# Optimization experiments

Hardware: AMD Instinct MI355X
Metric: run time of the kernel (lower is better)

Reference implementation:

```python
import jax, jax.numpy as jnp
import numpy as np

B, N = 2, 2048
D_MODEL, HEADS = 512, 8
D_K = D_MODEL // HEADS
D_HIDDEN = 2048
MIN_SPREAD = 2.0
MIN_RBF = 1e-3
MAX_RBF = 1.0
LN_EPS = 1e-5


def setup_inputs() -> dict:
    key = jax.random.key(0)
    ks = jax.random.split(key, 12)
    xs = (6.0 / (D_K + D_MODEL)) ** 0.5
    q = jax.random.normal(ks[0], (B, N, D_MODEL), dtype=jnp.float32)
    k = jax.random.normal(ks[1], (B, N, D_MODEL), dtype=jnp.float32)
    v = jax.random.normal(ks[2], (B, N, D_MODEL), dtype=jnp.float32)
    coords = jax.random.normal(ks[3], (B, N, 3), dtype=jnp.float32) * 10.0
    mask = jnp.ones((B, N), dtype=bool)
    q_proj = jax.random.uniform(ks[4], (HEADS, D_MODEL, D_K), minval=-xs, maxval=xs)
    k_proj = jax.random.uniform(ks[5], (HEADS, D_MODEL, D_K), minval=-xs, maxval=xs)
    v_proj = jax.random.uniform(ks[6], (HEADS, D_MODEL, D_K), minval=-xs, maxval=xs)
    q_bias = jnp.zeros((HEADS, D_K))
    k_bias = jnp.zeros((HEADS, D_K))
    v_bias = jnp.zeros((HEADS, D_K))
    ow = (1.0 / D_MODEL) ** 0.5
    out_w = jax.random.uniform(ks[7], (D_MODEL, D_MODEL), minval=-ow, maxval=ow)
    spread_w = jnp.zeros((HEADS,))
    beta_w = jnp.zeros((HEADS,))
    ln1_g = jnp.ones((D_MODEL,)); ln1_b = jnp.zeros((D_MODEL,))
    ln2_g = jnp.ones((D_MODEL,)); ln2_b = jnp.zeros((D_MODEL,))
    w1 = jax.random.normal(ks[8], (D_MODEL, D_HIDDEN)) * 0.02
    b1 = jnp.zeros((D_HIDDEN,))
    w2 = jax.random.normal(ks[9], (D_HIDDEN, D_MODEL)) * 0.02
    b2 = jnp.zeros((D_MODEL,))
    return dict(q=q, k=k, v=v, coords=coords, mask=mask,
                q_proj=q_proj, k_proj=k_proj, v_proj=v_proj,
                q_bias=q_bias, k_bias=k_bias, v_bias=v_bias,
                out_w=out_w, spread_w=spread_w, beta_w=beta_w,
                ln1_g=ln1_g, ln1_b=ln1_b, ln2_g=ln2_g, ln2_b=ln2_b,
                w1=w1, b1=b1, w2=w2, b2=b2)


def _layernorm(x, g, b):
    mu = jnp.mean(x, axis=-1, keepdims=True)
    var = jnp.mean((x - mu) ** 2, axis=-1, keepdims=True)
    return (x - mu) * jax.lax.rsqrt(var + LN_EPS) * g + b


def _geo_attention(q, k, v, coords, mask,
                   q_proj, k_proj, v_proj, q_bias, k_bias, v_bias,
                   out_w, spread_w, beta_w):
    # per-head projections: [B,H,N,dk]
    Q = jnp.einsum('bnd,hdk->bhnk', q, q_proj) + q_bias[None, :, None, :]
    K = jnp.einsum('bnd,hdk->bhnk', k, k_proj) + k_bias[None, :, None, :]
    V = jnp.einsum('bnd,hdk->bhnk', v, v_proj) + v_bias[None, :, None, :]

    spreads = MIN_SPREAD + jnp.exp(spread_w)   # [H]
    betas = jnp.exp(beta_w)                    # [H]

    # pairwise squared distances [B,N,N]
    d2 = jnp.sum((coords[:, :, None, :] - coords[:, None, :, :]) ** 2, axis=-1)
    # per-head Gaussian RBF [B,H,N,N]
    rbf = jnp.exp(-d2[:, None, :, :] / (2.0 * spreads[None, :, None, None] ** 2))

    scores = jnp.einsum('bhnk,bhmk->bhnm', Q, K) / jnp.sqrt(jnp.float32(D_K))
    scores = betas[None, :, None, None] * rbf * scores

    # sparsity: keys with rbf outside [min_rbf, max_rbf] or padded are masked out
    valid = (rbf >= MIN_RBF) & (rbf <= MAX_RBF) & mask[:, None, None, :]
    scores = jnp.where(valid, scores, -jnp.inf)
    attn = jax.nn.softmax(scores, axis=-1)     # diagonal always valid (rbf=1)

    out = jnp.einsum('bhnm,bhmk->bhnk', attn, V)         # [B,H,N,dk]
    # torch: out.permute(0,2,3,1).reshape(B,N,d_model) -> (b,n,dk,h) layout
    out = jnp.transpose(out, (0, 2, 3, 1)).reshape(out.shape[0], out.shape[2], D_MODEL)
    return out @ out_w.T


def reference(q, k, v, coords, mask,
              q_proj, k_proj, v_proj, q_bias, k_bias, v_bias,
              out_w, spread_w, beta_w,
              ln1_g, ln1_b, ln2_g, ln2_b, w1, b1, w2, b2):
    attn_out = _geo_attention(q, k, v, coords, mask,
                              q_proj, k_proj, v_proj, q_bias, k_bias, v_bias,
                              out_w, spread_w, beta_w)
    x = _layernorm(q + attn_out, ln1_g, ln1_b)
    ffn = jax.nn.relu(x @ w1 + b1) @ w2 + b2
    x = _layernorm(x + ffn, ln2_g, ln2_b)
    return x
```

## Files before the change

### kernel.cpp

```cpp
#include <hip/hip_runtime.h>
#include <math.h>

typedef __attribute__((ext_vector_type(8))) short bf16x8;
typedef __attribute__((ext_vector_type(4))) float f32x4;

#define MFMA16(a,b,c) __builtin_amdgcn_mfma_f32_16x16x32_bf16((a),(b),(c),0,0,0)

__device__ __forceinline__ unsigned short f2bf(float f) {
    union { float f; unsigned u; } x; x.f = f;
    unsigned r = x.u + 0x7FFFu + ((x.u >> 16) & 1u);
    return (unsigned short)(r >> 16);
}

__device__ __forceinline__ unsigned cvt_pk_bf16(float lo, float hi) {
    unsigned r;
    asm("v_cvt_pk_bf16_f32 %0, %1, %2" : "=v"(r) : "v"(lo), "v"(hi));
    return r;
}

__global__ __launch_bounds__(256) void cvt_qkv(
    const float* __restrict__ q, const float* __restrict__ k,
    const float* __restrict__ v,
    unsigned short* __restrict__ qb, unsigned short* __restrict__ kb,
    unsigned short* __restrict__ vb, int n)
{
    for (int i = blockIdx.x * 256 + threadIdx.x; i < n; i += gridDim.x * 256) {
        qb[i] = f2bf(q[i]); kb[i] = f2bf(k[i]); vb[i] = f2bf(v[i]);
    }
}

__global__ __launch_bounds__(256) void cvt_weights(
    const float* __restrict__ qp, const float* __restrict__ kp,
    const float* __restrict__ vp, const float* __restrict__ ow,
    const float* __restrict__ w1, const float* __restrict__ w2,
    unsigned short* __restrict__ qpT, unsigned short* __restrict__ kpT,
    unsigned short* __restrict__ vpT, unsigned short* __restrict__ owT,
    unsigned short* __restrict__ w1T, unsigned short* __restrict__ w2T)
{
    const int NP = 262144;
    const int total = 4 * NP + 1048576 + 1048576;
    for (int i = blockIdx.x * 256 + threadIdx.x; i < total; i += gridDim.x * 256) {
        if (i < 3 * NP) {
            int which = i / NP, r = i - which * NP;
            int n = r >> 9, d = r & 511;
            int h = n >> 6, kk = n & 63;
            const float* src = (which == 0) ? qp : (which == 1) ? kp : vp;
            unsigned short* dst = (which == 0) ? qpT : (which == 1) ? kpT : vpT;
            dst[r] = f2bf(src[(h << 15) + (d << 6) + kk]);
        } else if (i < 4 * NP) {
            int r = i - 3 * NP;
            int oi = r >> 9, f = r & 511;
            int h = f >> 6, kk = f & 63;
            owT[r] = f2bf(ow[(oi << 9) + (kk << 3) + h]);
        } else if (i < 4 * NP + 1048576) {
            int r = i - 4 * NP;
            int n = r >> 9, d = r & 511;
            w1T[r] = f2bf(w1[(d << 11) + n]);
        } else {
            int r = i - 4 * NP - 1048576;
            int n = r >> 11, d = r & 2047;
            w2T[r] = f2bf(w2[(d << 9) + n]);
        }
    }
}

template<int RELU, int SF32, int SB16, int SVTR>
__global__ __launch_bounds__(256) void gemm_bt(
    const unsigned short* __restrict__ A,
    const unsigned short* __restrict__ Bt,
    const float* __restrict__ bias,
    float* __restrict__ Cf, unsigned short* __restrict__ Cb,
    int M, int N, int K)
{
    __shared__ unsigned short As[128][72];
    __shared__ unsigned short Bs[128][72];
    const int tid = threadIdx.x;
    const int m0 = blockIdx.y << 7, n0 = blockIdx.x << 7;
    const int wv = tid >> 6, lane = tid & 63;
    const int lrow = lane & 15, kg = lane >> 4;
    const int wr = (wv >> 1) << 6, wc = (wv & 1) << 6;

    f32x4 acc[4][4];
    const f32x4 z4 = {0.f, 0.f, 0.f, 0.f};
#pragma unroll
    for (int i = 0; i < 4; ++i)
#pragma unroll
        for (int j = 0; j < 4; ++j) acc[i][j] = z4;

    const int nkt = K >> 6;
    for (int kt = 0; kt < nkt; ++kt) {
        __syncthreads();
        const int k0 = kt << 6;
#pragma unroll
        for (int i = 0; i < 4; ++i) {
            int slot = tid + (i << 8);
            int r = slot >> 3, c = (slot & 7) << 3;
            *(int4*)(&As[r][c]) = *(const int4*)(&A[(long)(m0 + r) * K + k0 + c]);
            *(int4*)(&Bs[r][c]) = *(const int4*)(&Bt[(long)(n0 + r) * K + k0 + c]);
        }
        __syncthreads();
#pragma unroll
        for (int ks = 0; ks < 2; ++ks) {
            const int koff = (ks << 5) + (kg << 3);
            bf16x8 af[4], bfr[4];
#pragma unroll
            for (int mi = 0; mi < 4; ++mi)
                af[mi] = *(const bf16x8*)(&As[wr + (mi << 4) + lrow][koff]);
#pragma unroll
            for (int ni = 0; ni < 4; ++ni)
                bfr[ni] = *(const bf16x8*)(&Bs[wc + (ni << 4) + lrow][koff]);
#pragma unroll
            for (int mi = 0; mi < 4; ++mi)
#pragma unroll
                for (int ni = 0; ni < 4; ++ni)
                    acc[mi][ni] = MFMA16(af[mi], bfr[ni], acc[mi][ni]);
        }
    }

#pragma unroll
    for (int mi = 0; mi < 4; ++mi) {
#pragma unroll
        for (int ni = 0; ni < 4; ++ni) {
            const int col = n0 + wc + (ni << 4) + lrow;
            const float bv = bias ? bias[col] : 0.0f;
#pragma unroll
            for (int j = 0; j < 4; ++j) {
                const int row = m0 + wr + (mi << 4) + (kg << 2) + j;
                float val = acc[mi][ni][j] + bv;
                if (RELU) val = fmaxf(val, 0.0f);
                if (SF32) Cf[(long)row * N + col] = val;
                if (SB16) Cb[(long)row * N + col] = f2bf(val);
                if (SVTR)
                    Cb[((long)(row >> 11) << 20) + ((long)col << 11) + (row & 2047)] = f2bf(val);
            }
        }
    }
}

__global__ __launch_bounds__(256) void geo_attn(
    const unsigned short* __restrict__ Qh,
    const unsigned short* __restrict__ Kh,
    const unsigned short* __restrict__ VhT,
    const float* __restrict__ coords,
    const float* __restrict__ spread_w, const float* __restrict__ beta_w,
    unsigned short* __restrict__ Ob)
{
    __shared__ unsigned short Qs[64][72];
    __shared__ unsigned short Ks[64][72];
    __shared__ unsigned short Vs[64][72];
    __shared__ unsigned short Ps[4][16][72];
    __shared__ float4 ck4[64];

    const int tid = threadIdx.x;
    const int bid = blockIdx.x;
    const int swz = ((bid & 7) << 6) + (bid >> 3);
    const int bh = swz >> 5, qt = swz & 31;
    const int b = bh >> 3, h = bh & 7;
    const int wv = tid >> 6, lane = tid & 63;
    const int lq = lane & 15, kg = lane >> 4;
    const float NEG_INF = -__builtin_inff();

    const float spread = 2.0f + __expf(spread_w[h]);
    const float inv2s2 = 1.0f / (2.0f * spread * spread);
    const float coef = __expf(beta_w[h]) * 0.125f;

    {
        const long qbase = ((long)(b * 2048 + qt * 64)) * 512 + h * 64;
#pragma unroll
        for (int i = 0; i < 2; ++i) {
            int slot = tid + (i << 8);
            int r = slot >> 3, c = (slot & 7) << 3;
            *(int4*)(&Qs[r][c]) = *(const int4*)(&Qh[qbase + (long)r * 512 + c]);
        }
    }

    float cqx, cqy, cqz;
    {
        long ca = ((long)(b * 2048 + qt * 64 + wv * 16 + lq)) * 3;
        cqx = coords[ca]; cqy = coords[ca + 1]; cqz = coords[ca + 2];
    }

    float mrun = NEG_INF, lrun = 0.0f;
    f32x4 Oa[4];
    const f32x4 z4 = {0.f, 0.f, 0.f, 0.f};
#pragma unroll
    for (int nd = 0; nd < 4; ++nd) Oa[nd] = z4;

    const long kbase0 = ((long)b * 2048) * 512 + h * 64;
    const long vbase = ((long)(b * 8 + h)) * 131072;

    for (int kt = 0; kt < 32; ++kt) {
        __syncthreads();
        const int k0 = kt << 6;
#pragma unroll
        for (int i = 0; i < 2; ++i) {
            int slot = tid + (i << 8);
            int r = slot >> 3, c = (slot & 7) << 3;
            *(int4*)(&Ks[r][c]) = *(const int4*)(&Kh[kbase0 + (long)(k0 + r) * 512 + c]);
            *(int4*)(&Vs[r][c]) = *(const int4*)(&VhT[vbase + (long)r * 2048 + k0 + c]);
        }
        if (tid < 64) {
            long ca = ((long)(b * 2048 + k0 + tid)) * 3;
            ck4[tid] = make_float4(coords[ca], coords[ca + 1], coords[ca + 2], 0.0f);
        }
        __syncthreads();

        f32x4 t4[4];
#pragma unroll
        for (int ra = 0; ra < 4; ++ra) t4[ra] = z4;
#pragma unroll
        for (int ks = 0; ks < 2; ++ks) {
            const int koff = (ks << 5) + (kg << 3);
            bf16x8 bq = *(const bf16x8*)(&Qs[(wv << 4) + lq][koff]);
#pragma unroll
            for (int ra = 0; ra < 4; ++ra) {
                bf16x8 ak = *(const bf16x8*)(&Ks[(ra << 4) + lq][koff]);
                t4[ra] = MFMA16(ak, bq, t4[ra]);
            }
        }

        float tmax = NEG_INF;
#pragma unroll
        for (int ra = 0; ra < 4; ++ra) {
#pragma unroll
            for (int j = 0; j < 4; ++j) {
                float4 ck = ck4[(ra << 4) + (kg << 2) + j];
                float dx = cqx - ck.x, dy = cqy - ck.y, dz = cqz - ck.z;
                float d2 = dx * dx + dy * dy + dz * dz;
                float rbf = __expf(-d2 * inv2s2);
                float val = (rbf >= 1e-3f) ? coef * rbf * t4[ra][j] : NEG_INF;
                t4[ra][j] = val;
                tmax = fmaxf(tmax, val);
            }
        }
        tmax = fmaxf(tmax, __shfl_xor(tmax, 16, 64));
        tmax = fmaxf(tmax, __shfl_xor(tmax, 32, 64));

        const float mn = fmaxf(mrun, tmax);
        const bool dead = (mn == NEG_INF);
        const float mneff = dead ? 0.0f : mn;
        const float fcorr = dead ? 1.0f : __expf(mrun - mn);

        float psum = 0.0f;
#pragma unroll
        for (int ra = 0; ra < 4; ++ra) {
#pragma unroll
            for (int j = 0; j < 4; ++j) {
                float p = __expf(t4[ra][j] - mneff);
                t4[ra][j] = p;
                psum += p;
            }
        }
        psum += __shfl_xor(psum, 16, 64);
        psum += __shfl_xor(psum, 32, 64);
        mrun = mn;
        lrun = lrun * fcorr + psum;

#pragma unroll
        for (int ra = 0; ra < 4; ++ra) {
            uint2 pk;
            pk.x = cvt_pk_bf16(t4[ra][0], t4[ra][1]);
            pk.y = cvt_pk_bf16(t4[ra][2], t4[ra][3]);
            *(uint2*)(&Ps[wv][lq][(ra << 4) + (kg << 2)]) = pk;
        }

        float fb[4];
#pragma unroll
        for (int j = 0; j < 4; ++j)
            fb[j] = __shfl(fcorr, (lane & 48) | ((kg << 2) + j), 64);
#pragma unroll
        for (int nd = 0; nd < 4; ++nd)
#pragma unroll
            for (int j = 0; j < 4; ++j)
                Oa[nd][j] *= fb[j];

#pragma unroll
        for (int ks = 0; ks < 2; ++ks) {
            const int koff = (ks << 5) + (kg << 3);
            bf16x8 ap = *(const bf16x8*)(&Ps[wv][lq][koff]);
#pragma unroll
            for (int nd = 0; nd < 4; ++nd) {
                bf16x8 bv = *(const bf16x8*)(&Vs[(nd << 4) + lq][koff]);
                Oa[nd] = MFMA16(ap, bv, Oa[nd]);
            }
        }
    }

    const float inv = 1.0f / lrun;
    float il[4];
#pragma unroll
    for (int j = 0; j < 4; ++j)
        il[j] = __shfl(inv, (lane & 48) | ((kg << 2) + j), 64);
    const long obase = ((long)(b * 2048 + qt * 64 + (wv << 4))) * 512 + h * 64;
#pragma unroll
    for (int nd = 0; nd < 4; ++nd)
#pragma unroll
        for (int j = 0; j < 4; ++j)
            Ob[obase + (long)((kg << 2) + j) * 512 + (nd << 4) + lq] =
                f2bf(Oa[nd][j] * il[j]);
}

template<int SB16>
__global__ __launch_bounds__(256) void ln_res(
    const float* __restrict__ X, const float* __restrict__ R,
    const float* __restrict__ g, const float* __restrict__ bb,
    float* __restrict__ Yf, unsigned short* __restrict__ Yb)
{
    const int wv = threadIdx.x >> 6, lane = threadIdx.x & 63;
    const long row = (long)blockIdx.x * 4 + wv;
    const float* xp = X + row * 512;
    const float* rp = R + row * 512;
    const int c0 = lane * 8;
    float4 a0 = *(const float4*)(xp + c0);
    float4 a1 = *(const float4*)(xp + c0 + 4);
    float4 r0 = *(const float4*)(rp + c0);
    float4 r1 = *(const float4*)(rp + c0 + 4);
    float v[8] = {a0.x + r0.x, a0.y + r0.y, a0.z + r0.z, a0.w + r0.w,
                  a1.x + r1.x, a1.y + r1.y, a1.z + r1.z, a1.w + r1.w};
    float s = 0.f, ss = 0.f;
#pragma unroll
    for (int i = 0; i < 8; ++i) { s += v[i]; ss += v[i] * v[i]; }
#pragma unroll
    for (int off = 1; off < 64; off <<= 1) {
        s += __shfl_xor(s, off, 64);
        ss += __shfl_xor(ss, off, 64);
    }
    const float mu = s * (1.0f / 512.0f);
    const float var = ss * (1.0f / 512.0f) - mu * mu;
    const float rstd = rsqrtf(var + 1e-5f);
#pragma unroll
    for (int i = 0; i < 8; ++i) {
        const int c = c0 + i;
        const float y = (v[i] - mu) * rstd * g[c] + bb[c];
        Yf[row * 512 + c] = y;
        if (SB16) Yb[row * 512 + c] = f2bf(y);
    }
}

extern "C" void kernel_launch(void* const* d_in, const int* in_sizes, int n_in,
                              void* d_out, int out_size, void* d_ws, size_t ws_size,
                              hipStream_t stream)
{
    const float* q      = (const float*)d_in[0];
    const float* k      = (const float*)d_in[1];
    const float* v      = (const float*)d_in[2];
    const float* coords = (const float*)d_in[3];
    const float* q_proj = (const float*)d_in[5];
    const float* k_proj = (const float*)d_in[6];
    const float* v_proj = (const float*)d_in[7];
    const float* q_bias = (const float*)d_in[8];
    const float* k_bias = (const float*)d_in[9];
    const float* v_bias = (const float*)d_in[10];
    const float* out_w  = (const float*)d_in[11];
    const float* spread_w = (const float*)d_in[12];
    const float* beta_w = (const float*)d_in[13];
    const float* ln1_g  = (const float*)d_in[14];
    const float* ln1_b  = (const float*)d_in[15];
    const float* ln2_g  = (const float*)d_in[16];
    const float* ln2_b  = (const float*)d_in[17];
    const float* w1     = (const float*)d_in[18];
    const float* b1     = (const float*)d_in[19];
    const float* w2     = (const float*)d_in[20];
    const float* b2     = (const float*)d_in[21];
    float* out = (float*)d_out;

    char* ws = (char*)d_ws;
    size_t off = 0;
    auto alloc = [&](size_t bytes) -> void* {
        void* p = ws + off;
        off += (bytes + 255) & ~(size_t)255;
        return p;
    };
    unsigned short* qb   = (unsigned short*)alloc(4096UL * 512 * 2);
    unsigned short* kb   = (unsigned short*)alloc(4096UL * 512 * 2);
    unsigned short* vb   = (unsigned short*)alloc(4096UL * 512 * 2);
    unsigned short* qpT  = (unsigned short*)alloc(512UL * 512 * 2);
    unsigned short* kpT  = (unsigned short*)alloc(512UL * 512 * 2);
    unsigned short* vpT  = (unsigned short*)alloc(512UL * 512 * 2);
    unsigned short* owT  = (unsigned short*)alloc(512UL * 512 * 2);
    unsigned short* w1T  = (unsigned short*)alloc(2048UL * 512 * 2);
    unsigned short* w2T  = (unsigned short*)alloc(512UL * 2048 * 2);
    unsigned short* Qp   = (unsigned short*)alloc(4096UL * 512 * 2);
    unsigned short* Kp   = (unsigned short*)alloc(4096UL * 512 * 2);
    unsigned short* VpT  = (unsigned short*)alloc(4096UL * 512 * 2);
    unsigned short* attnb= (unsigned short*)alloc(4096UL * 512 * 2);
    float* proj = (float*)alloc(4096UL * 512 * 4);
    float* x1   = (float*)alloc(4096UL * 512 * 4);
    unsigned short* x1b = (unsigned short*)alloc(4096UL * 512 * 2);
    unsigned short* hid = (unsigned short*)alloc(4096UL * 2048 * 2);
    float* ffn  = (float*)alloc(4096UL * 512 * 4);
    (void)ws_size; (void)in_sizes; (void)n_in; (void)out_size;

    cvt_qkv<<<2048, 256, 0, stream>>>(q, k, v, qb, kb, vb, 2097152);
    cvt_weights<<<2048, 256, 0, stream>>>(q_proj, k_proj, v_proj, out_w, w1, w2,
                                          qpT, kpT, vpT, owT, w1T, w2T);

    dim3 g512(4, 32);
    gemm_bt<0, 0, 1, 0><<<g512, 256, 0, stream>>>(qb, qpT, q_bias, nullptr, Qp, 4096, 512, 512);
    gemm_bt<0, 0, 1, 0><<<g512, 256, 0, stream>>>(kb, kpT, k_bias, nullptr, Kp, 4096, 512, 512);
    gemm_bt<0, 0, 0, 1><<<g512, 256, 0, stream>>>(vb, vpT, v_bias, nullptr, VpT, 4096, 512, 512);

    geo_attn<<<512, 256, 0, stream>>>(Qp, Kp, VpT, coords, spread_w, beta_w, attnb);

    gemm_bt<0, 1, 0, 0><<<g512, 256, 0, stream>>>(attnb, owT, nullptr, proj, nullptr, 4096, 512, 512);
    ln_res<1><<<1024, 256, 0, stream>>>(proj, q, ln1_g, ln1_b, x1, x1b);

    dim3 g2048(16, 32);
    gemm_bt<1, 0, 1, 0><<<g2048, 256, 0, stream>>>(x1b, w1T, b1, nullptr, hid, 4096, 2048, 512);
    gemm_bt<0, 1, 0, 0><<<g512, 256, 0, stream>>>(hid, w2T, b2, ffn, nullptr, 4096, 512, 2048);
    ln_res<0><<<1024, 256, 0, stream>>>(ffn, x1, ln2_g, ln2_b, out, nullptr);
}
```

Baseline: 229.6 us.

## Fuse fp32-to-bf16 input conversion into GEMMs, add register prefetch, widen attention tiles

Drops the separate q/k/v conversion kernel. The projection GEMMs now read fp32 activations directly and convert them while staging into shared memory. GEMM and attention loops prefetch the next tile into registers while computing on the current one. The GEMM M-tile becomes a template parameter, set to 64 for the 512-wide GEMMs to launch more blocks. Attention processes 128 keys per iteration with Q held in registers, halving the loop count, at the cost of more registers and LDS, which may lower occupancy.

```diff
diff --git a/kernel.cpp b/kernel.cpp
--- a/kernel.cpp
+++ b/kernel.cpp
@@ -16,17 +16,6 @@
     unsigned r;
     asm("v_cvt_pk_bf16_f32 %0, %1, %2" : "=v"(r) : "v"(lo), "v"(hi));
     return r;
-}
-
-__global__ __launch_bounds__(256) void cvt_qkv(
-    const float* __restrict__ q, const float* __restrict__ k,
-    const float* __restrict__ v,
-    unsigned short* __restrict__ qb, unsigned short* __restrict__ kb,
-    unsigned short* __restrict__ vb, int n)
-{
-    for (int i = blockIdx.x * 256 + threadIdx.x; i < n; i += gridDim.x * 256) {
-        qb[i] = f2bf(q[i]); kb[i] = f2bf(k[i]); vb[i] = f2bf(v[i]);
-    }
 }
 
 __global__ __launch_bounds__(256) void cvt_weights(
@@ -64,61 +53,105 @@
     }
 }
 
-template<int RELU, int SF32, int SB16, int SVTR>
+template<int TM, int AF32, int RELU, int SF32, int SB16, int SVTR>
 __global__ __launch_bounds__(256) void gemm_bt(
-    const unsigned short* __restrict__ A,
+    const void* __restrict__ Av,
     const unsigned short* __restrict__ Bt,
     const float* __restrict__ bias,
     float* __restrict__ Cf, unsigned short* __restrict__ Cb,
     int M, int N, int K)
 {
-    __shared__ unsigned short As[128][72];
+    constexpr int AC = TM / 32;
+    __shared__ unsigned short As[TM][72];
     __shared__ unsigned short Bs[128][72];
     const int tid = threadIdx.x;
-    const int m0 = blockIdx.y << 7, n0 = blockIdx.x << 7;
+    const int m0 = blockIdx.y * TM, n0 = blockIdx.x << 7;
     const int wv = tid >> 6, lane = tid & 63;
     const int lrow = lane & 15, kg = lane >> 4;
-    const int wr = (wv >> 1) << 6, wc = (wv & 1) << 6;
-
-    f32x4 acc[4][4];
+    const int wr = (wv >> 1) * (TM / 2), wc = (wv & 1) << 6;
+
+    f32x4 acc[AC][4];
     const f32x4 z4 = {0.f, 0.f, 0.f, 0.f};
 #pragma unroll
-    for (int i = 0; i < 4; ++i)
+    for (int i = 0; i < AC; ++i)
 #pragma unroll
         for (int j = 0; j < 4; ++j) acc[i][j] = z4;
 
+    float4 arf[AC][2];
+    int4 arb[AC];
+    int4 br[4];
+
+    auto loadT = [&](int kt) {
+        const int k0 = kt << 6;
+#pragma unroll
+        for (int i = 0; i < AC; ++i) {
+            int slot = tid + (i << 8);
+            int r = slot >> 3, c = (slot & 7) << 3;
+            if (AF32) {
+                const float* Af = (const float*)Av;
+                arf[i][0] = *(const float4*)(&Af[(long)(m0 + r) * K + k0 + c]);
+                arf[i][1] = *(const float4*)(&Af[(long)(m0 + r) * K + k0 + c + 4]);
+            } else {
+                const unsigned short* Ab = (const unsigned short*)Av;
+                arb[i] = *(const int4*)(&Ab[(long)(m0 + r) * K + k0 + c]);
+            }
+        }
+#pragma unroll
+        for (int i = 0; i < 4; ++i) {
+            int slot = tid + (i << 8);
+            int r = slot >> 3, c = (slot & 7) << 3;
+            br[i] = *(const int4*)(&Bt[(long)(n0 + r) * K + k0 + c]);
+        }
+    };
+    auto writeT = [&]() {
+#pragma unroll
+        for (int i = 0; i < AC; ++i) {
+            int slot = tid + (i << 8);
+            int r = slot >> 3, c = (slot & 7) << 3;
+            if (AF32) {
+                int4 w;
+                w.x = (int)cvt_pk_bf16(arf[i][0].x, arf[i][0].y);
+                w.y = (int)cvt_pk_bf16(arf[i][0].z, arf[i][0].w);
+                w.z = (int)cvt_pk_bf16(arf[i][1].x, arf[i][1].y);
+                w.w = (int)cvt_pk_bf16(arf[i][1].z, arf[i][1].w);
+                *(int4*)(&As[r][c]) = w;
+            } else {
+                *(int4*)(&As[r][c]) = arb[i];
+            }
+        }
+#pragma unroll
+        for (int i = 0; i < 4; ++i) {
+            int slot = tid + (i << 8);
+            *(int4*)(&Bs[slot >> 3][(slot & 7) << 3]) = br[i];
+        }
+    };
+
     const int nkt = K >> 6;
+    loadT(0); writeT(); __syncthreads();
+
     for (int kt = 0; kt < nkt; ++kt) {
-        __syncthreads();
-        const int k0 = kt << 6;
-#pragma unroll
-        for (int i = 0; i < 4; ++i) {
-            int slot = tid + (i << 8);
-            int r = slot >> 3, c = (slot & 7) << 3;
-            *(int4*)(&As[r][c]) = *(const int4*)(&A[(long)(m0 + r) * K + k0 + c]);
-            *(int4*)(&Bs[r][c]) = *(const int4*)(&Bt[(long)(n0 + r) * K + k0 + c]);
-        }
-        __syncthreads();
+        if (kt + 1 < nkt) loadT(kt + 1);
 #pragma unroll
         for (int ks = 0; ks < 2; ++ks) {
             const int koff = (ks << 5) + (kg << 3);
-            bf16x8 af[4], bfr[4];
-#pragma unroll
-            for (int mi = 0; mi < 4; ++mi)
+            bf16x8 af[AC], bfr[4];
+#pragma unroll
+            for (int mi = 0; mi < AC; ++mi)
                 af[mi] = *(const bf16x8*)(&As[wr + (mi << 4) + lrow][koff]);
 #pragma unroll
             for (int ni = 0; ni < 4; ++ni)
                 bfr[ni] = *(const bf16x8*)(&Bs[wc + (ni << 4) + lrow][koff]);
 #pragma unroll
-            for (int mi = 0; mi < 4; ++mi)
+            for (int mi = 0; mi < AC; ++mi)
 #pragma unroll
                 for (int ni = 0; ni < 4; ++ni)
                     acc[mi][ni] = MFMA16(af[mi], bfr[ni], acc[mi][ni]);
         }
-    }
-
-#pragma unroll
-    for (int mi = 0; mi < 4; ++mi) {
+        if (kt + 1 < nkt) { __syncthreads(); writeT(); __syncthreads(); }
+    }
+
+#pragma unroll
+    for (int mi = 0; mi < AC; ++mi) {
 #pragma unroll
         for (int ni = 0; ni < 4; ++ni) {
             const int col = n0 + wc + (ni << 4) + lrow;
@@ -145,11 +178,10 @@
     const float* __restrict__ spread_w, const float* __restrict__ beta_w,
     unsigned short* __restrict__ Ob)
 {
-    __shared__ unsigned short Qs[64][72];
-    __shared__ unsigned short Ks[64][72];
-    __shared__ unsigned short Vs[64][72];
-    __shared__ unsigned short Ps[4][16][72];
-    __shared__ float4 ck4[64];
+    __shared__ unsigned short Ks[128][72];
+    __shared__ unsigned short Vs[64][136];
+    __shared__ unsigned short Ps[4][16][136];
+    __shared__ float4 ck4[128];
 
     const int tid = threadIdx.x;
     const int bid = blockIdx.x;
@@ -164,21 +196,11 @@
     const float inv2s2 = 1.0f / (2.0f * spread * spread);
     const float coef = __expf(beta_w[h]) * 0.125f;
 
-    {
-        const long qbase = ((long)(b * 2048 + qt * 64)) * 512 + h * 64;
-#pragma unroll
-        for (int i = 0; i < 2; ++i) {
-            int slot = tid + (i << 8);
-            int r = slot >> 3, c = (slot & 7) << 3;
-            *(int4*)(&Qs[r][c]) = *(const int4*)(&Qh[qbase + (long)r * 512 + c]);
-        }
-    }
-
+    const long qrow = (long)(b * 2048 + qt * 64 + wv * 16 + lq);
+    const bf16x8 qA = *(const bf16x8*)(&Qh[qrow * 512 + h * 64 + (kg << 3)]);
+    const bf16x8 qB = *(const bf16x8*)(&Qh[qrow * 512 + h * 64 + 32 + (kg << 3)]);
     float cqx, cqy, cqz;
-    {
-        long ca = ((long)(b * 2048 + qt * 64 + wv * 16 + lq)) * 3;
-        cqx = coords[ca]; cqy = coords[ca + 1]; cqz = coords[ca + 2];
-    }
+    { long ca = qrow * 3; cqx = coords[ca]; cqy = coords[ca + 1]; cqz = coords[ca + 2]; }
 
     float mrun = NEG_INF, lrun = 0.0f;
     f32x4 Oa[4];
@@ -189,31 +211,48 @@
     const long kbase0 = ((long)b * 2048) * 512 + h * 64;
     const long vbase = ((long)(b * 8 + h)) * 131072;
 
-    for (int kt = 0; kt < 32; ++kt) {
-        __syncthreads();
-        const int k0 = kt << 6;
-#pragma unroll
-        for (int i = 0; i < 2; ++i) {
-            int slot = tid + (i << 8);
-            int r = slot >> 3, c = (slot & 7) << 3;
-            *(int4*)(&Ks[r][c]) = *(const int4*)(&Kh[kbase0 + (long)(k0 + r) * 512 + c]);
-            *(int4*)(&Vs[r][c]) = *(const int4*)(&VhT[vbase + (long)r * 2048 + k0 + c]);
-        }
-        if (tid < 64) {
+    int4 kr[4], vr[4];
+    float c0r = 0.f, c1r = 0.f, c2r = 0.f;
+
+    auto loadTile = [&](int kt) {
+        const int k0 = kt << 7;
+#pragma unroll
+        for (int i = 0; i < 4; ++i) {
+            int slot = tid + (i << 8);
+            int krow = slot >> 3, kc = (slot & 7) << 3;
+            kr[i] = *(const int4*)(&Kh[kbase0 + (long)(k0 + krow) * 512 + kc]);
+            int vrow = slot >> 4, vc = (slot & 15) << 3;
+            vr[i] = *(const int4*)(&VhT[vbase + (long)vrow * 2048 + k0 + vc]);
+        }
+        if (tid < 128) {
             long ca = ((long)(b * 2048 + k0 + tid)) * 3;
-            ck4[tid] = make_float4(coords[ca], coords[ca + 1], coords[ca + 2], 0.0f);
-        }
-        __syncthreads();
-
-        f32x4 t4[4];
-#pragma unroll
-        for (int ra = 0; ra < 4; ++ra) t4[ra] = z4;
+            c0r = coords[ca]; c1r = coords[ca + 1]; c2r = coords[ca + 2];
+        }
+    };
+    auto writeTile = [&]() {
+#pragma unroll
+        for (int i = 0; i < 4; ++i) {
+            int slot = tid + (i << 8);
+            *(int4*)(&Ks[slot >> 3][(slot & 7) << 3]) = kr[i];
+            *(int4*)(&Vs[slot >> 4][(slot & 15) << 3]) = vr[i];
+        }
+        if (tid < 128) ck4[tid] = make_float4(c0r, c1r, c2r, 0.0f);
+    };
+
+    loadTile(0); writeTile(); __syncthreads();
+
+    for (int kt = 0; kt < 16; ++kt) {
+        if (kt + 1 < 16) loadTile(kt + 1);
+
+        f32x4 t4[8];
+#pragma unroll
+        for (int ra = 0; ra < 8; ++ra) t4[ra] = z4;
 #pragma unroll
         for (int ks = 0; ks < 2; ++ks) {
             const int koff = (ks << 5) + (kg << 3);
-            bf16x8 bq = *(const bf16x8*)(&Qs[(wv << 4) + lq][koff]);
-#pragma unroll
-            for (int ra = 0; ra < 4; ++ra) {
+            const bf16x8 bq = ks ? qB : qA;
+#pragma unroll
+            for (int ra = 0; ra < 8; ++ra) {
                 bf16x8 ak = *(const bf16x8*)(&Ks[(ra << 4) + lq][koff]);
                 t4[ra] = MFMA16(ak, bq, t4[ra]);
             }
@@ -221,7 +260,7 @@
 
         float tmax = NEG_INF;
 #pragma unroll
-        for (int ra = 0; ra < 4; ++ra) {
+        for (int ra = 0; ra < 8; ++ra) {
 #pragma unroll
             for (int j = 0; j < 4; ++j) {
                 float4 ck = ck4[(ra << 4) + (kg << 2) + j];
@@ -243,7 +282,7 @@
 
         float psum = 0.0f;
 #pragma unroll
-        for (int ra = 0; ra < 4; ++ra) {
+        for (int ra = 0; ra < 8; ++ra) {
 #pragma unroll
             for (int j = 0; j < 4; ++j) {
                 float p = __expf(t4[ra][j] - mneff);
@@ -257,7 +296,7 @@
         lrun = lrun * fcorr + psum;
 
 #pragma unroll
-        for (int ra = 0; ra < 4; ++ra) {
+        for (int ra = 0; ra < 8; ++ra) {
             uint2 pk;
             pk.x = cvt_pk_bf16(t4[ra][0], t4[ra][1]);
             pk.y = cvt_pk_bf16(t4[ra][2], t4[ra][3]);
@@ -275,7 +314,7 @@
                 Oa[nd][j] *= fb[j];
 
 #pragma unroll
-        for (int ks = 0; ks < 2; ++ks) {
+        for (int ks = 0; ks < 4; ++ks) {
             const int koff = (ks << 5) + (kg << 3);
             bf16x8 ap = *(const bf16x8*)(&Ps[wv][lq][koff]);
 #pragma unroll
@@ -284,6 +323,8 @@
                 Oa[nd] = MFMA16(ap, bv, Oa[nd]);
             }
         }
+
+        if (kt + 1 < 16) { __syncthreads(); writeTile(); __syncthreads(); }
     }
 
     const float inv = 1.0f / lrun;
@@ -371,9 +412,6 @@
         off += (bytes + 255) & ~(size_t)255;
         return p;
     };
-    unsigned short* qb   = (unsigned short*)alloc(4096UL * 512 * 2);
-    unsigned short* kb   = (unsigned short*)alloc(4096UL * 512 * 2);
-    unsigned short* vb   = (unsigned short*)alloc(4096UL * 512 * 2);
     unsigned short* qpT  = (unsigned short*)alloc(512UL * 512 * 2);
     unsigned short* kpT  = (unsigned short*)alloc(512UL * 512 * 2);
     unsigned short* vpT  = (unsigned short*)alloc(512UL * 512 * 2);
@@ -391,22 +429,21 @@
     float* ffn  = (float*)alloc(4096UL * 512 * 4);
     (void)ws_size; (void)in_sizes; (void)n_in; (void)out_size;
 
-    cvt_qkv<<<2048, 256, 0, stream>>>(q, k, v, qb, kb, vb, 2097152);
     cvt_weights<<<2048, 256, 0, stream>>>(q_proj, k_proj, v_proj, out_w, w1, w2,
                                           qpT, kpT, vpT, owT, w1T, w2T);
 
-    dim3 g512(4, 32);
-    gemm_bt<0, 0, 1, 0><<<g512, 256, 0, stream>>>(qb, qpT, q_bias, nullptr, Qp, 4096, 512, 512);
-    gemm_bt<0, 0, 1, 0><<<g512, 256, 0, stream>>>(kb, kpT, k_bias, nullptr, Kp, 4096, 512, 512);
-    gemm_bt<0, 0, 0, 1><<<g512, 256, 0, stream>>>(vb, vpT, v_bias, nullptr, VpT, 4096, 512, 512);
+    dim3 g64(4, 64);
+    gemm_bt<64, 1, 0, 0, 1, 0><<<g64, 256, 0, stream>>>(q, qpT, q_bias, nullptr, Qp, 4096, 512, 512);
+    gemm_bt<64, 1, 0, 0, 1, 0><<<g64, 256, 0, stream>>>(k, kpT, k_bias, nullptr, Kp, 4096, 512, 512);
+    gemm_bt<64, 1, 0, 0, 0, 1><<<g64, 256, 0, stream>>>(v, vpT, v_bias, nullptr, VpT, 4096, 512, 512);
 
     geo_attn<<<512, 256, 0, stream>>>(Qp, Kp, VpT, coords, spread_w, beta_w, attnb);
 
-    gemm_bt<0, 1, 0, 0><<<g512, 256, 0, stream>>>(attnb, owT, nullptr, proj, nullptr, 4096, 512, 512);
+    gemm_bt<64, 0, 0, 1, 0, 0><<<g64, 256, 0, stream>>>(attnb, owT, nullptr, proj, nullptr, 4096, 512, 512);
     ln_res<1><<<1024, 256, 0, stream>>>(proj, q, ln1_g, ln1_b, x1, x1b);
 
     dim3 g2048(16, 32);
-    gemm_bt<1, 0, 1, 0><<<g2048, 256, 0, stream>>>(x1b, w1T, b1, nullptr, hid, 4096, 2048, 512);
-    gemm_bt<0, 1, 0, 0><<<g512, 256, 0, stream>>>(hid, w2T, b2, ffn, nullptr, 4096, 512, 2048);
+    gemm_bt<128, 0, 1, 0, 1, 0><<<g2048, 256, 0, stream>>>(x1b, w1T, b1, nullptr, hid, 4096, 2048, 512);
+    gemm_bt<64, 0, 0, 1, 0, 0><<<g64, 256, 0, stream>>>(hid, w2T, b2, ffn, nullptr, 4096, 512, 2048);
     ln_res<0><<<1024, 256, 0, stream>>>(ffn, x1, ln2_g, ln2_b, out, nullptr);
 }
```

Measured after the change: 313.1 us. 1.36x slower.
